# Performance work log

Hardware: AMD Instinct MI355X
Metric: run time of the kernel (lower is better)

The kernel has to match this reference:

```python
import jax, jax.numpy as jnp
import numpy as np

D_MODEL = 768
N_HEADS = 8
HEAD_DIM = D_MODEL // N_HEADS
LN_EPS = 1e-5

def setup_inputs() -> dict:
    key = jax.random.key(0)
    k1, k2, k3 = jax.random.split(key, 3)
    B, L = 8, 4096
    x = jax.random.normal(k1, (B, L, D_MODEL), dtype=jnp.float32)
    gamma = jnp.ones((D_MODEL,), dtype=jnp.float32)
    beta = jnp.zeros((D_MODEL,), dtype=jnp.float32)
    # torch Linear weights transposed so forward is x @ W
    w_qkv = jax.random.normal(k2, (D_MODEL, 3 * D_MODEL), dtype=jnp.float32) * (1.0 / np.sqrt(D_MODEL))
    w_out = jax.random.normal(k3, (D_MODEL, D_MODEL), dtype=jnp.float32) * (1.0 / np.sqrt(D_MODEL))
    return {"x": x, "gamma": gamma, "beta": beta, "w_qkv": w_qkv, "w_out": w_out}

def reference(x, gamma, beta, w_qkv, w_out):
    B, L, D = x.shape
    residual = x
    # LayerNorm
    mu = jnp.mean(x, axis=-1, keepdims=True)
    var = jnp.mean(jnp.square(x - mu), axis=-1, keepdims=True)
    xn = (x - mu) * jax.lax.rsqrt(var + LN_EPS) * gamma + beta
    # qkv projection, split, reshape to [B, H, L, d]
    qkv = xn @ w_qkv  # [B, L, 3D]
    q, k, v = jnp.split(qkv, 3, axis=-1)
    def to_heads(t):
        return t.reshape(B, L, N_HEADS, HEAD_DIM).transpose(0, 2, 1, 3)
    q, k, v = to_heads(q), to_heads(k), to_heads(v)
    # feature maps: elu + 1
    q = jax.nn.elu(q) + 1.0
    k = jax.nn.elu(k) + 1.0
    # linear attention: kv aggregation then query readout
    kv = jnp.einsum('bhld,bhlv->bhdv', k, v)          # [B,H,d,d]
    out = jnp.einsum('bhld,bhdv->bhlv', q, kv)         # [B,H,L,d]
    k_sum = jnp.sum(k, axis=2)                         # [B,H,d]
    normalizer = jnp.einsum('bhld,bhd->bhl', q, k_sum) # [B,H,L]
    normalizer = jnp.maximum(normalizer, 1e-6)
    out = out / normalizer[..., None]
    out = out.transpose(0, 2, 1, 3).reshape(B, L, D)
    out = out @ w_out
    return out + residual
```

## Files before the change

### kernel.cpp

```cpp
#include <hip/hip_runtime.h>
#include <stdint.h>

#define D_MODEL 768
#define N3      2304
#define NHEAD   8
#define DH      96
#define BATCH   8
#define SEQ     4096
#define ROWS    (BATCH*SEQ)
#define LN_EPS  1e-5f

typedef __attribute__((ext_vector_type(8))) __bf16 bf16x8;
typedef __attribute__((ext_vector_type(4))) float f32x4;
typedef __attribute__((ext_vector_type(8))) unsigned short ushort8;
typedef __attribute__((ext_vector_type(4))) unsigned short ushort4v;

__device__ __forceinline__ unsigned short f2bf(float f) {
  union { float f; unsigned int u; } v; v.f = f;
  unsigned int r = v.u + 0x7FFFu + ((v.u >> 16) & 1u);
  return (unsigned short)(r >> 16);
}
__device__ __forceinline__ float bf2f(unsigned short u) {
  union { unsigned int u; float f; } v; v.u = ((unsigned int)u) << 16;
  return v.f;
}

#define GLOBAL_LDS16(src, dst) \
  __builtin_amdgcn_global_load_lds((const __attribute__((address_space(1))) void*)(src), \
                                   (__attribute__((address_space(3))) void*)(dst), 16, 0, 0)

#define GATE(n) do { asm volatile("s_waitcnt vmcnt(" #n ")" ::: "memory"); \
                     __builtin_amdgcn_s_barrier(); asm volatile("" ::: "memory"); } while (0)

__global__ __launch_bounds__(256) void transpose2_kernel(
    const float* __restrict__ wqkv, const float* __restrict__ wout,
    unsigned short* __restrict__ wqkvT, unsigned short* __restrict__ woutT) {
  __shared__ float tile[32][33];
  int bx = blockIdx.x;
  const float* in; unsigned short* out; int C, c0;
  if (bx < 72) { in = wqkv; out = wqkvT; C = N3;      c0 = bx * 32; }
  else         { in = wout; out = woutT; C = D_MODEL; c0 = (bx - 72) * 32; }
  int r0 = blockIdx.y * 32;
  int tx = threadIdx.x & 31, ty = threadIdx.x >> 5;
  #pragma unroll
  for (int i = ty; i < 32; i += 8)
    tile[i][tx] = in[(size_t)(r0 + i) * C + c0 + tx];
  __syncthreads();
  #pragma unroll
  for (int i = ty; i < 32; i += 8)
    out[(size_t)(c0 + i) * D_MODEL + r0 + tx] = f2bf(tile[tx][i]);
}

__global__ __launch_bounds__(256) void ln_kernel(
    const float* __restrict__ x, const float* __restrict__ gamma,
    const float* __restrict__ beta, unsigned short* __restrict__ xn) {
  int wave = threadIdx.x >> 6, lane = threadIdx.x & 63;
  int row = blockIdx.x * 4 + wave;
  const float* xr = x + (size_t)row * D_MODEL;
  f32x4 v[3];
  float s = 0.f, sq = 0.f;
  #pragma unroll
  for (int i = 0; i < 3; ++i) {
    v[i] = *(const f32x4*)(xr + (i * 64 + lane) * 4);
    #pragma unroll
    for (int c = 0; c < 4; ++c) { s += v[i][c]; sq += v[i][c] * v[i][c]; }
  }
  #pragma unroll
  for (int o = 32; o; o >>= 1) {
    s  += __shfl_xor(s, o, 64);
    sq += __shfl_xor(sq, o, 64);
  }
  float mu  = s * (1.f / 768.f);
  float var = sq * (1.f / 768.f) - mu * mu;
  float rs  = rsqrtf(var + LN_EPS);
  #pragma unroll
  for (int i = 0; i < 3; ++i) {
    int col = (i * 64 + lane) * 4;
    ushort4v o;
    #pragma unroll
    for (int c = 0; c < 4; ++c)
      o[c] = f2bf((v[i][c] - mu) * rs * gamma[col + c] + beta[col + c]);
    *(ushort4v*)(xn + (size_t)row * D_MODEL + col) = o;
  }
}

__global__ __launch_bounds__(256, 2) void gemm_qkv_w_kernel(
    const unsigned short* __restrict__ A, const unsigned short* __restrict__ Bt,
    unsigned short* __restrict__ qb, unsigned short* __restrict__ kT,
    unsigned short* __restrict__ vT) {
  __shared__ unsigned short As[3 * 4096];
  __shared__ unsigned short Bs[3 * 8192];
  const int K = D_MODEL, nbn = 9;
  int nwg = gridDim.x, id = blockIdx.x;
  int q8 = nwg >> 3;
  int wg = (id & 7) * q8 + (id >> 3);
  int bm = wg / nbn, bn = wg % nbn;

  const int lane = threadIdx.x & 63, wid = threadIdx.x >> 6;
  const int wn = wid;
  const int l15 = lane & 15, hi = lane >> 4;
  const int colS = (hi ^ ((l15 >> 1) & 3)) << 3;
  const int srow = lane >> 2;
  const int scol = ((lane & 3) ^ ((lane >> 3) & 3)) << 3;

  const unsigned short* a0 = A  + (size_t)(bm * 128 +      wid * 16 + srow) * K + scol;
  const unsigned short* a1 = A  + (size_t)(bm * 128 + 64 + wid * 16 + srow) * K + scol;
  const unsigned short* b0 = Bt + (size_t)(bn * 256 + wid * 64 +      srow) * K + scol;
  const unsigned short* b1 = Bt + (size_t)(bn * 256 + wid * 64 + 16 + srow) * K + scol;
  const unsigned short* b2 = Bt + (size_t)(bn * 256 + wid * 64 + 32 + srow) * K + scol;
  const unsigned short* b3 = Bt + (size_t)(bn * 256 + wid * 64 + 48 + srow) * K + scol;
  auto stage = [&](int buf, int kt) {
    GLOBAL_LDS16(a0 + kt * 32, &As[buf * 4096 +        wid * 512]);
    GLOBAL_LDS16(a1 + kt * 32, &As[buf * 4096 + 2048 + wid * 512]);
    GLOBAL_LDS16(b0 + kt * 32, &Bs[buf * 8192 + wid * 2048]);
    GLOBAL_LDS16(b1 + kt * 32, &Bs[buf * 8192 + wid * 2048 + 512]);
    GLOBAL_LDS16(b2 + kt * 32, &Bs[buf * 8192 + wid * 2048 + 1024]);
    GLOBAL_LDS16(b3 + kt * 32, &Bs[buf * 8192 + wid * 2048 + 1536]);
  };

  f32x4 acc[8][4];
  #pragma unroll
  for (int i = 0; i < 8; ++i)
    #pragma unroll
    for (int j = 0; j < 4; ++j) acc[i][j] = (f32x4){0.f, 0.f, 0.f, 0.f};

#define QTILE(BUF, STG) do { \
    bf16x8 af[8], bv[4]; \
    _Pragma("unroll") for (int mf = 0; mf < 8; ++mf) \
      af[mf] = *(const bf16x8*)&As[(BUF) * 4096 + (mf * 16 + l15) * 32 + colS]; \
    _Pragma("unroll") for (int nf = 0; nf < 4; ++nf) \
      bv[nf] = *(const bf16x8*)&Bs[(BUF) * 8192 + (wn * 64 + nf * 16 + l15) * 32 + colS]; \
    STG; \
    __builtin_amdgcn_s_setprio(1); \
    _Pragma("unroll") for (int mf = 0; mf < 8; ++mf) \
      _Pragma("unroll") for (int nf = 0; nf < 4; ++nf) \
        acc[mf][nf] = __builtin_amdgcn_mfma_f32_16x16x32_bf16( \
            af[mf], bv[nf], acc[mf][nf], 0, 0, 0); \
    __builtin_amdgcn_s_setprio(0); \
  } while (0)

  stage(0, 0); stage(1, 1);
  for (int it = 0; it < 7; ++it) {
    int T = 3 * it;
    GATE(6); QTILE(0, stage(2, T + 2));
    GATE(6); QTILE(1, stage(0, T + 3));
    GATE(6); QTILE(2, stage(1, T + 4));
  }
  GATE(6); QTILE(0, stage(2, 23));
  GATE(6); QTILE(1, {});
  GATE(0); QTILE(2, {});
#undef QTILE

  int r0 = bm * 128, c0 = bn * 256 + wn * 64;
  if (bn < 3) {
    #pragma unroll
    for (int mf = 0; mf < 8; ++mf)
      #pragma unroll
      for (int nf = 0; nf < 4; ++nf) {
        int col = c0 + nf * 16 + l15;
        #pragma unroll
        for (int r = 0; r < 4; ++r) {
          int row = r0 + mf * 16 + hi * 4 + r;
          float v = acc[mf][nf][r];
          v = (v > 0.f) ? v + 1.f : __expf(v);
          qb[(size_t)row * D_MODEL + col] = f2bf(v);
        }
      }
  } else {
    const bool isK = (bn < 6);
    unsigned short* T = isK ? kT : vT;
    int cbase = c0 - (isK ? 768 : 1536);
    #pragma unroll
    for (int mf = 0; mf < 8; ++mf) {
      int ll = mf * 16 + hi * 4;
      #pragma unroll
      for (int nf = 0; nf < 4; ++nf) {
        int cc = cbase + nf * 16 + l15;
        int h = cc / 96, d = cc - h * 96;
        ushort4v pk;
        #pragma unroll
        for (int r = 0; r < 4; ++r) {
          float v = acc[mf][nf][r];
          if (isK) v = (v > 0.f) ? v + 1.f : __expf(v);
          pk[r] = f2bf(v);
        }
        *(ushort4v*)&T[(((size_t)bm * 8 + h) * 96 + d) * 128 + ll] = pk;
      }
    }
  }
}

__global__ __launch_bounds__(256, 3) void gemm_out_kernel(
    const unsigned short* __restrict__ A, const unsigned short* __restrict__ Bt,
    const float* __restrict__ resid, float* __restrict__ Cf) {
  __shared__ unsigned short As[3 * 4096];
  __shared__ unsigned short Bs[3 * 4096];
  const int K = D_MODEL, nbn = 6;
  int nwg = gridDim.x, id = blockIdx.x;
  int q8 = nwg >> 3;
  int wg = (id & 7) * q8 + (id >> 3);
  int bm = wg / nbn, bn = wg % nbn;

  const int lane = threadIdx.x & 63, wid = threadIdx.x >> 6;
  const int wm = wid >> 1, wn = wid & 1;
  const int l15 = lane & 15, hi = lane >> 4;
  const int colS = (hi ^ ((l15 >> 1) & 3)) << 3;
  const int srow = lane >> 2;
  const int scol = ((lane & 3) ^ ((lane >> 3) & 3)) << 3;

  const unsigned short* a0 = A  + (size_t)(bm * 128 +      wid * 16 + srow) * K + scol;
  const unsigned short* a1 = A  + (size_t)(bm * 128 + 64 + wid * 16 + srow) * K + scol;
  const unsigned short* b0 = Bt + (size_t)(bn * 128 +      wid * 16 + srow) * K + scol;
  const unsigned short* b1 = Bt + (size_t)(bn * 128 + 64 + wid * 16 + srow) * K + scol;
  auto stage = [&](int buf, int kt) {
    GLOBAL_LDS16(a0 + kt * 32, &As[buf * 4096 +        wid * 512]);
    GLOBAL_LDS16(a1 + kt * 32, &As[buf * 4096 + 2048 + wid * 512]);
    GLOBAL_LDS16(b0 + kt * 32, &Bs[buf * 4096 +        wid * 512]);
    GLOBAL_LDS16(b1 + kt * 32, &Bs[buf * 4096 + 2048 + wid * 512]);
  };

  f32x4 acc[4][4];
  #pragma unroll
  for (int i = 0; i < 4; ++i)
    #pragma unroll
    for (int j = 0; j < 4; ++j) acc[i][j] = (f32x4){0.f, 0.f, 0.f, 0.f};

#define HTILE(BUF, STG) do { \
    bf16x8 af[4], bv[4]; \
    _Pragma("unroll") for (int mf = 0; mf < 4; ++mf) \
      af[mf] = *(const bf16x8*)&As[(BUF) * 4096 + (wm * 64 + mf * 16 + l15) * 32 + colS]; \
    _Pragma("unroll") for (int nf = 0; nf < 4; ++nf) \
      bv[nf] = *(const bf16x8*)&Bs[(BUF) * 4096 + (wn * 64 + nf * 16 + l15) * 32 + colS]; \
    STG; \
    __builtin_amdgcn_s_setprio(1); \
    _Pragma("unroll") for (int mf = 0; mf < 4; ++mf) \
      _Pragma("unroll") for (int nf = 0; nf < 4; ++nf) \
        acc[mf][nf] = __builtin_amdgcn_mfma_f32_16x16x32_bf16( \
            af[mf], bv[nf], acc[mf][nf], 0, 0, 0); \
    __builtin_amdgcn_s_setprio(0); \
  } while (0)

  stage(0, 0); stage(1, 1);
  for (int it = 0; it < 7; ++it) {
    int T = 3 * it;
    GATE(4); HTILE(0, stage(2, T + 2));
    GATE(4); HTILE(1, stage(0, T + 3));
    GATE(4); HTILE(2, stage(1, T + 4));
  }
  GATE(4); HTILE(0, stage(2, 23));
  GATE(4); HTILE(1, {});
  GATE(0); HTILE(2, {});
#undef HTILE

  int r0 = bm * 128 + wm * 64, c0 = bn * 128 + wn * 64;
  #pragma unroll
  for (int mf = 0; mf < 4; ++mf)
    #pragma unroll
    for (int nf = 0; nf < 4; ++nf) {
      int col = c0 + nf * 16 + l15;
      #pragma unroll
      for (int r = 0; r < 4; ++r) {
        int row = r0 + mf * 16 + hi * 4 + r;
        Cf[(size_t)row * D_MODEL + col] =
            acc[mf][nf][r] + resid[(size_t)row * D_MODEL + col];
      }
    }
}

__global__ __launch_bounds__(256) void kvagg2_kernel(
    const unsigned short* __restrict__ kT, const unsigned short* __restrict__ vT,
    float* __restrict__ kvp) {
  __shared__ unsigned short KTs[3 * 6144];
  __shared__ unsigned short VTs[3 * 8192];
  int bh = blockIdx.x >> 2, chunk = blockIdx.x & 3;
  int tid = threadIdx.x;
  int lane = tid & 63, wid = tid >> 6;
  int l15 = lane & 15, hi = lane >> 4;

  #pragma unroll
  for (int i = 0; i < 3; ++i) {
    int s = i * 256 + tid;
    int buf = s >> 8, r = 96 + ((s >> 3) & 31), sl = s & 7;
    unsigned short val = (r == 96) ? (unsigned short)0x3F80 : (unsigned short)0;
    ushort8 v8 = {val, val, val, val, val, val, val, val};
    *(ushort8*)&VTs[buf * 8192 + r * 64 + sl * 8] = v8;
  }
  __syncthreads();

  const int b = bh >> 3, h = bh & 7;
  auto stage = [&](int buf, int t) {
    #pragma unroll
    for (int i = 0; i < 3; ++i) {
      int sidx = i * 256 + tid;
      int row = sidx >> 3;
      int L = (sidx & 7) ^ (row & 7);
      size_t g = ((((size_t)b * 32 + chunk * 8 + (t >> 1)) * 8 + h) * 96 + row) * 128
               + (t & 1) * 64 + L * 8;
      GLOBAL_LDS16(kT + g, &KTs[buf * 6144 + (i * 256 + wid * 64) * 8]);
      GLOBAL_LDS16(vT + g, &VTs[buf * 8192 + (i * 256 + wid * 64) * 8]);
    }
  };

  f32x4 acc[6][2];
  #pragma unroll
  for (int i = 0; i < 6; ++i)
    #pragma unroll
    for (int j = 0; j < 2; ++j) acc[i][j] = (f32x4){0.f, 0.f, 0.f, 0.f};

#define KVTILE(BUF) do { \
    _Pragma("unroll") for (int kq = 0; kq < 2; ++kq) { \
      bf16x8 af[6], bv[2]; \
      _Pragma("unroll") for (int mf = 0; mf < 6; ++mf) { \
        int row = mf * 16 + l15; \
        af[mf] = *(const bf16x8*)&KTs[(BUF) * 6144 + row * 64 + ((kq * 4 + hi) ^ (row & 7)) * 8]; } \
      _Pragma("unroll") for (int nf = 0; nf < 2; ++nf) { \
        int row = wid * 32 + nf * 16 + l15; \
        bv[nf] = *(const bf16x8*)&VTs[(BUF) * 8192 + row * 64 + ((kq * 4 + hi) ^ (row & 7)) * 8]; } \
      __builtin_amdgcn_s_setprio(1); \
      _Pragma("unroll") for (int mf = 0; mf < 6; ++mf) \
        _Pragma("unroll") for (int nf = 0; nf < 2; ++nf) \
          acc[mf][nf] = __builtin_amdgcn_mfma_f32_16x16x32_bf16( \
              af[mf], bv[nf], acc[mf][nf], 0, 0, 0); \
      __builtin_amdgcn_s_setprio(0); \
    } } while (0)

  stage(0, 0); stage(1, 1);
  for (int t = 0; t < 14; ++t) {
    stage((t + 2) % 3, t + 2);
    GATE(12);
    KVTILE(t % 3);
  }
  GATE(6); KVTILE(2);
  GATE(0); KVTILE(0);
#undef KVTILE

  float* outp = kvp + ((size_t)bh * 4 + chunk) * (96 * 112);
  #pragma unroll
  for (int nf = 0; nf < 2; ++nf) {
    int e = wid * 32 + nf * 16 + l15;
    if (e < 112) {
      #pragma unroll
      for (int mf = 0; mf < 6; ++mf)
        #pragma unroll
        for (int r = 0; r < 4; ++r) {
          int d = mf * 16 + hi * 4 + r;
          outp[d * 112 + e] = acc[mf][nf][r];
        }
    }
  }
}

__global__ __launch_bounds__(256) void kvreduce_kernel(
    const float* __restrict__ kvp, unsigned short* __restrict__ kvTo) {
  int idx = blockIdx.x * 256 + threadIdx.x;
  if (idx >= 64 * 112 * 96) return;
  int d = idx % 96;
  int e = (idx / 96) % 112;
  int bh = idx / (96 * 112);
  float s = 0.f;
  #pragma unroll
  for (int c = 0; c < 4; ++c)
    s += kvp[(((size_t)bh * 4 + c) * 96 + d) * 112 + e];
  kvTo[idx] = f2bf(s);
}

__global__ __launch_bounds__(256) void readout_kernel(
    const unsigned short* __restrict__ qb, const unsigned short* __restrict__ kvT,
    unsigned short* __restrict__ attn) {
  __shared__ unsigned short Qs[128][104];
  __shared__ unsigned short Ks[112][104];
  int bh = blockIdx.x >> 5, lc = blockIdx.x & 31;
  int b = bh >> 3, h = bh & 7;
  int l0 = lc * 128;
  int wave = threadIdx.x >> 6, lane = threadIdx.x & 63;
  #pragma unroll
  for (int i = 0; i < 6; ++i) {
    int idx = i * 256 + threadIdx.x;
    int l = idx / 12, oc = idx % 12;
    size_t g = ((size_t)b * SEQ + l0 + l) * D_MODEL + h * DH + oc * 8;
    *(ushort8*)&Qs[l][oc * 8] = *(const ushort8*)(qb + g);
  }
  const unsigned short* kvbh = kvT + (size_t)bh * 112 * 96;
  #pragma unroll
  for (int i = 0; i < 6; ++i) {
    int idx = i * 256 + threadIdx.x;
    if (idx < 1344) {
      int e = idx / 12, oc = idx % 12;
      *(ushort8*)&Ks[e][oc * 8] = *(const ushort8*)(kvbh + e * 96 + oc * 8);
    }
  }
  __syncthreads();
  f32x4 acc[2][7];
  #pragma unroll
  for (int i = 0; i < 2; ++i)
    #pragma unroll
    for (int j = 0; j < 7; ++j) acc[i][j] = (f32x4){0.f, 0.f, 0.f, 0.f};
  #pragma unroll
  for (int kq = 0; kq < 3; ++kq) {
    int k0 = kq * 32 + (lane >> 4) * 8;
    bf16x8 af[2], bfv[7];
    #pragma unroll
    for (int i = 0; i < 2; ++i) af[i]  = *(const bf16x8*)&Qs[wave * 32 + i * 16 + (lane & 15)][k0];
    #pragma unroll
    for (int j = 0; j < 7; ++j) bfv[j] = *(const bf16x8*)&Ks[j * 16 + (lane & 15)][k0];
    #pragma unroll
    for (int i = 0; i < 2; ++i)
      #pragma unroll
      for (int j = 0; j < 7; ++j)
        acc[i][j] = __builtin_amdgcn_mfma_f32_16x16x32_bf16(af[i], bfv[j], acc[i][j], 0, 0, 0);
  }
  int g4 = lane >> 4;
  #pragma unroll
  for (int i = 0; i < 2; ++i) {
    #pragma unroll
    for (int r = 0; r < 4; ++r) {
      float nv = __shfl(acc[i][6][r], lane & 48, 64);
      float inv = 1.f / fmaxf(nv, 1e-6f);
      size_t orow = (size_t)b * SEQ + l0 + wave * 32 + i * 16 + g4 * 4 + r;
      #pragma unroll
      for (int j = 0; j < 6; ++j) {
        int col = h * DH + j * 16 + (lane & 15);
        attn[orow * D_MODEL + col] = f2bf(acc[i][j][r] * inv);
      }
    }
  }
}

extern "C" void kernel_launch(void* const* d_in, const int* in_sizes, int n_in,
                              void* d_out, int out_size, void* d_ws, size_t ws_size,
                              hipStream_t stream) {
  const float* x     = (const float*)d_in[0];
  const float* gamma = (const float*)d_in[1];
  const float* beta  = (const float*)d_in[2];
  const float* w_qkv = (const float*)d_in[3];
  const float* w_out = (const float*)d_in[4];
  float* out = (float*)d_out;

  char* ws = (char*)d_ws;
  size_t off = 0;
  auto alloc = [&](size_t bytes) -> void* {
    void* p = ws + off; off += (bytes + 255) & ~(size_t)255; return p;
  };
  unsigned short* xn    = (unsigned short*)alloc((size_t)ROWS * D_MODEL * 2);
  unsigned short* qb    = (unsigned short*)alloc((size_t)ROWS * D_MODEL * 2);
  unsigned short* kTb   = (unsigned short*)alloc((size_t)64 * 96 * SEQ * 2);
  unsigned short* vTb   = (unsigned short*)alloc((size_t)64 * 96 * SEQ * 2);
  unsigned short* wqkvT = (unsigned short*)alloc((size_t)N3 * D_MODEL * 2);
  unsigned short* woutT = (unsigned short*)alloc((size_t)D_MODEL * D_MODEL * 2);
  float* kvp            = (float*)alloc((size_t)256 * 96 * 112 * 4);
  unsigned short* kvT   = (unsigned short*)alloc((size_t)64 * 112 * 96 * 2);

  transpose2_kernel<<<dim3(96, 24), 256, 0, stream>>>(w_qkv, w_out, wqkvT, woutT);
  ln_kernel<<<ROWS / 4, 256, 0, stream>>>(x, gamma, beta, xn);
  gemm_qkv_w_kernel<<<(ROWS / 128) * (N3 / 256), 256, 0, stream>>>(xn, wqkvT, qb, kTb, vTb);
  kvagg2_kernel<<<256, 256, 0, stream>>>(kTb, vTb, kvp);
  kvreduce_kernel<<<(64 * 112 * 96 + 255) / 256, 256, 0, stream>>>(kvp, kvT);
  readout_kernel<<<2048, 256, 0, stream>>>(qb, kvT, xn);
  gemm_out_kernel<<<(ROWS / 128) * (D_MODEL / 128), 256, 0, stream>>>(xn, woutT, x, out);
}
```

Before: 326.0 us.

## Fold kv state into output projection per batch, replacing readout GEMM

The per-head kv matrices are premultiplied with the output projection weights, giving a per-batch 768x768 matrix M. Queries are then scaled by their normalizer in a lightweight elementwise kernel, and one GEMM per batch (q_hat @ M + residual) replaces the separate readout GEMM and output GEMM. This removes one full pass over the attention intermediate and the readout MFMA work. In exchange it adds a small premultiply kernel and an extra bf16 rounding of the normalized queries and of M. The final GEMM also moves to a larger 128x256 tile at lower occupancy.

```diff
diff --git a/kernel.cpp b/kernel.cpp
--- a/kernel.cpp
+++ b/kernel.cpp
@@ -188,83 +188,6 @@
       }
     }
   }
-}
-
-__global__ __launch_bounds__(256, 3) void gemm_out_kernel(
-    const unsigned short* __restrict__ A, const unsigned short* __restrict__ Bt,
-    const float* __restrict__ resid, float* __restrict__ Cf) {
-  __shared__ unsigned short As[3 * 4096];
-  __shared__ unsigned short Bs[3 * 4096];
-  const int K = D_MODEL, nbn = 6;
-  int nwg = gridDim.x, id = blockIdx.x;
-  int q8 = nwg >> 3;
-  int wg = (id & 7) * q8 + (id >> 3);
-  int bm = wg / nbn, bn = wg % nbn;
-
-  const int lane = threadIdx.x & 63, wid = threadIdx.x >> 6;
-  const int wm = wid >> 1, wn = wid & 1;
-  const int l15 = lane & 15, hi = lane >> 4;
-  const int colS = (hi ^ ((l15 >> 1) & 3)) << 3;
-  const int srow = lane >> 2;
-  const int scol = ((lane & 3) ^ ((lane >> 3) & 3)) << 3;
-
-  const unsigned short* a0 = A  + (size_t)(bm * 128 +      wid * 16 + srow) * K + scol;
-  const unsigned short* a1 = A  + (size_t)(bm * 128 + 64 + wid * 16 + srow) * K + scol;
-  const unsigned short* b0 = Bt + (size_t)(bn * 128 +      wid * 16 + srow) * K + scol;
-  const unsigned short* b1 = Bt + (size_t)(bn * 128 + 64 + wid * 16 + srow) * K + scol;
-  auto stage = [&](int buf, int kt) {
-    GLOBAL_LDS16(a0 + kt * 32, &As[buf * 4096 +        wid * 512]);
-    GLOBAL_LDS16(a1 + kt * 32, &As[buf * 4096 + 2048 + wid * 512]);
-    GLOBAL_LDS16(b0 + kt * 32, &Bs[buf * 4096 +        wid * 512]);
-    GLOBAL_LDS16(b1 + kt * 32, &Bs[buf * 4096 + 2048 + wid * 512]);
-  };
-
-  f32x4 acc[4][4];
-  #pragma unroll
-  for (int i = 0; i < 4; ++i)
-    #pragma unroll
-    for (int j = 0; j < 4; ++j) acc[i][j] = (f32x4){0.f, 0.f, 0.f, 0.f};
-
-#define HTILE(BUF, STG) do { \
-    bf16x8 af[4], bv[4]; \
-    _Pragma("unroll") for (int mf = 0; mf < 4; ++mf) \
-      af[mf] = *(const bf16x8*)&As[(BUF) * 4096 + (wm * 64 + mf * 16 + l15) * 32 + colS]; \
-    _Pragma("unroll") for (int nf = 0; nf < 4; ++nf) \
-      bv[nf] = *(const bf16x8*)&Bs[(BUF) * 4096 + (wn * 64 + nf * 16 + l15) * 32 + colS]; \
-    STG; \
-    __builtin_amdgcn_s_setprio(1); \
-    _Pragma("unroll") for (int mf = 0; mf < 4; ++mf) \
-      _Pragma("unroll") for (int nf = 0; nf < 4; ++nf) \
-        acc[mf][nf] = __builtin_amdgcn_mfma_f32_16x16x32_bf16( \
-            af[mf], bv[nf], acc[mf][nf], 0, 0, 0); \
-    __builtin_amdgcn_s_setprio(0); \
-  } while (0)
-
-  stage(0, 0); stage(1, 1);
-  for (int it = 0; it < 7; ++it) {
-    int T = 3 * it;
-    GATE(4); HTILE(0, stage(2, T + 2));
-    GATE(4); HTILE(1, stage(0, T + 3));
-    GATE(4); HTILE(2, stage(1, T + 4));
-  }
-  GATE(4); HTILE(0, stage(2, 23));
-  GATE(4); HTILE(1, {});
-  GATE(0); HTILE(2, {});
-#undef HTILE
-
-  int r0 = bm * 128 + wm * 64, c0 = bn * 128 + wn * 64;
-  #pragma unroll
-  for (int mf = 0; mf < 4; ++mf)
-    #pragma unroll
-    for (int nf = 0; nf < 4; ++nf) {
-      int col = c0 + nf * 16 + l15;
-      #pragma unroll
-      for (int r = 0; r < 4; ++r) {
-        int row = r0 + mf * 16 + hi * 4 + r;
-        Cf[(size_t)row * D_MODEL + col] =
-            acc[mf][nf][r] + resid[(size_t)row * D_MODEL + col];
-      }
-    }
 }
 
 __global__ __launch_bounds__(256) void kvagg2_kernel(
@@ -350,80 +273,196 @@
   }
 }
 
-__global__ __launch_bounds__(256) void kvreduce_kernel(
-    const float* __restrict__ kvp, unsigned short* __restrict__ kvTo) {
+__global__ __launch_bounds__(256) void kvreduce2_kernel(
+    const float* __restrict__ kvp, unsigned short* __restrict__ kvN,
+    float* __restrict__ ksumf) {
   int idx = blockIdx.x * 256 + threadIdx.x;
-  if (idx >= 64 * 112 * 96) return;
-  int d = idx % 96;
-  int e = (idx / 96) % 112;
-  int bh = idx / (96 * 112);
+  if (idx >= 64 * 96 * 112) return;
+  int e = idx % 112;
+  int d = (idx / 112) % 96;
+  int bh = idx / (112 * 96);
   float s = 0.f;
   #pragma unroll
   for (int c = 0; c < 4; ++c)
     s += kvp[(((size_t)bh * 4 + c) * 96 + d) * 112 + e];
-  kvTo[idx] = f2bf(s);
-}
-
-__global__ __launch_bounds__(256) void readout_kernel(
-    const unsigned short* __restrict__ qb, const unsigned short* __restrict__ kvT,
-    unsigned short* __restrict__ attn) {
-  __shared__ unsigned short Qs[128][104];
-  __shared__ unsigned short Ks[112][104];
-  int bh = blockIdx.x >> 5, lc = blockIdx.x & 31;
-  int b = bh >> 3, h = bh & 7;
-  int l0 = lc * 128;
-  int wave = threadIdx.x >> 6, lane = threadIdx.x & 63;
-  #pragma unroll
-  for (int i = 0; i < 6; ++i) {
-    int idx = i * 256 + threadIdx.x;
-    int l = idx / 12, oc = idx % 12;
-    size_t g = ((size_t)b * SEQ + l0 + l) * D_MODEL + h * DH + oc * 8;
-    *(ushort8*)&Qs[l][oc * 8] = *(const ushort8*)(qb + g);
-  }
-  const unsigned short* kvbh = kvT + (size_t)bh * 112 * 96;
-  #pragma unroll
-  for (int i = 0; i < 6; ++i) {
-    int idx = i * 256 + threadIdx.x;
-    if (idx < 1344) {
-      int e = idx / 12, oc = idx % 12;
-      *(ushort8*)&Ks[e][oc * 8] = *(const ushort8*)(kvbh + e * 96 + oc * 8);
-    }
+  if (e < 96)       kvN[((size_t)bh * 96 + d) * 96 + e] = f2bf(s);
+  else if (e == 96) ksumf[(size_t)bh * 96 + d] = s;
+}
+
+__global__ __launch_bounds__(256) void mpre_kernel(
+    const unsigned short* __restrict__ kvN, const unsigned short* __restrict__ woutT,
+    unsigned short* __restrict__ Mt) {
+  int bx = blockIdx.x;
+  int cb = bx % 3, h = (bx / 3) % 8, b = bx / 24;
+  int bh = b * 8 + h;
+  const int lane = threadIdx.x & 63, wid = threadIdx.x >> 6;
+  const int l15 = lane & 15, hi = lane >> 4;
+
+  f32x4 acc[6][4];
+  #pragma unroll
+  for (int i = 0; i < 6; ++i)
+    #pragma unroll
+    for (int j = 0; j < 4; ++j) acc[i][j] = (f32x4){0.f, 0.f, 0.f, 0.f};
+
+  #pragma unroll
+  for (int kq = 0; kq < 3; ++kq) {
+    int e = kq * 32 + hi * 8;
+    bf16x8 af[6], bv[4];
+    #pragma unroll
+    for (int rf = 0; rf < 6; ++rf) {
+      int d = rf * 16 + l15;
+      af[rf] = *(const bf16x8*)&kvN[((size_t)bh * 96 + d) * 96 + e];
+    }
+    #pragma unroll
+    for (int cf = 0; cf < 4; ++cf) {
+      int c = cb * 256 + wid * 64 + cf * 16 + l15;
+      bv[cf] = *(const bf16x8*)&woutT[(size_t)c * 768 + h * 96 + e];
+    }
+    #pragma unroll
+    for (int rf = 0; rf < 6; ++rf)
+      #pragma unroll
+      for (int cf = 0; cf < 4; ++cf)
+        acc[rf][cf] = __builtin_amdgcn_mfma_f32_16x16x32_bf16(
+            af[rf], bv[cf], acc[rf][cf], 0, 0, 0);
+  }
+
+  #pragma unroll
+  for (int rf = 0; rf < 6; ++rf) {
+    int hd = h * 96 + rf * 16 + hi * 4;
+    #pragma unroll
+    for (int cf = 0; cf < 4; ++cf) {
+      int c = cb * 256 + wid * 64 + cf * 16 + l15;
+      ushort4v pk;
+      #pragma unroll
+      for (int r = 0; r < 4; ++r) pk[r] = f2bf(acc[rf][cf][r]);
+      *(ushort4v*)&Mt[(size_t)b * 589824 + (size_t)c * 768 + hd] = pk;
+    }
+  }
+}
+
+__global__ __launch_bounds__(256) void scale_kernel(
+    const unsigned short* __restrict__ qb, const float* __restrict__ ksumf,
+    unsigned short* __restrict__ qhat) {
+  __shared__ float ks[8][96];
+  int tid = threadIdx.x;
+  int row0 = blockIdx.x * 64;
+  int b = row0 >> 12;
+  #pragma unroll
+  for (int i = 0; i < 3; ++i) {
+    int idx = i * 256 + tid;
+    if (idx < 768) ks[idx / 96][idx % 96] = ksumf[(size_t)b * 768 + idx];
   }
   __syncthreads();
-  f32x4 acc[2][7];
-  #pragma unroll
-  for (int i = 0; i < 2; ++i)
-    #pragma unroll
-    for (int j = 0; j < 7; ++j) acc[i][j] = (f32x4){0.f, 0.f, 0.f, 0.f};
-  #pragma unroll
-  for (int kq = 0; kq < 3; ++kq) {
-    int k0 = kq * 32 + (lane >> 4) * 8;
-    bf16x8 af[2], bfv[7];
-    #pragma unroll
-    for (int i = 0; i < 2; ++i) af[i]  = *(const bf16x8*)&Qs[wave * 32 + i * 16 + (lane & 15)][k0];
-    #pragma unroll
-    for (int j = 0; j < 7; ++j) bfv[j] = *(const bf16x8*)&Ks[j * 16 + (lane & 15)][k0];
-    #pragma unroll
-    for (int i = 0; i < 2; ++i)
-      #pragma unroll
-      for (int j = 0; j < 7; ++j)
-        acc[i][j] = __builtin_amdgcn_mfma_f32_16x16x32_bf16(af[i], bfv[j], acc[i][j], 0, 0, 0);
-  }
-  int g4 = lane >> 4;
-  #pragma unroll
-  for (int i = 0; i < 2; ++i) {
-    #pragma unroll
-    for (int r = 0; r < 4; ++r) {
-      float nv = __shfl(acc[i][6][r], lane & 48, 64);
-      float inv = 1.f / fmaxf(nv, 1e-6f);
-      size_t orow = (size_t)b * SEQ + l0 + wave * 32 + i * 16 + g4 * 4 + r;
-      #pragma unroll
-      for (int j = 0; j < 6; ++j) {
-        int col = h * DH + j * 16 + (lane & 15);
-        attn[orow * D_MODEL + col] = f2bf(acc[i][j][r] * inv);
+
+  int row = row0 + (tid >> 2), seg = tid & 3;
+  size_t base = (size_t)row * D_MODEL + seg * 192;
+  ushort8 qreg[24];
+  #pragma unroll
+  for (int c = 0; c < 24; ++c)
+    qreg[c] = *(const ushort8*)(qb + base + c * 8);
+
+  float inv[2];
+  #pragma unroll
+  for (int hh = 0; hh < 2; ++hh) {
+    int h = seg * 2 + hh;
+    float n = 0.f;
+    #pragma unroll
+    for (int c = 0; c < 12; ++c)
+      #pragma unroll
+      for (int j = 0; j < 8; ++j)
+        n += bf2f(qreg[hh * 12 + c][j]) * ks[h][c * 8 + j];
+    inv[hh] = 1.f / fmaxf(n, 1e-6f);
+  }
+  #pragma unroll
+  for (int c = 0; c < 24; ++c) {
+    float sc = inv[c / 12];
+    ushort8 o;
+    #pragma unroll
+    for (int j = 0; j < 8; ++j) o[j] = f2bf(bf2f(qreg[c][j]) * sc);
+    *(ushort8*)(qhat + base + c * 8) = o;
+  }
+}
+
+__global__ __launch_bounds__(256, 2) void gemm_fin_kernel(
+    const unsigned short* __restrict__ A, const unsigned short* __restrict__ MtAll,
+    const float* __restrict__ resid, float* __restrict__ Cf) {
+  __shared__ unsigned short As[3 * 4096];
+  __shared__ unsigned short Bs[3 * 8192];
+  const int K = D_MODEL, nbn = 3;
+  int nwg = gridDim.x, id = blockIdx.x;
+  int q8 = nwg >> 3;
+  int wg = (id & 7) * q8 + (id >> 3);
+  int bm = wg / nbn, bn = wg % nbn;
+  const unsigned short* Bt = MtAll + (size_t)(bm >> 5) * 589824;
+
+  const int lane = threadIdx.x & 63, wid = threadIdx.x >> 6;
+  const int wn = wid;
+  const int l15 = lane & 15, hi = lane >> 4;
+  const int colS = (hi ^ ((l15 >> 1) & 3)) << 3;
+  const int srow = lane >> 2;
+  const int scol = ((lane & 3) ^ ((lane >> 3) & 3)) << 3;
+
+  const unsigned short* a0 = A  + (size_t)(bm * 128 +      wid * 16 + srow) * K + scol;
+  const unsigned short* a1 = A  + (size_t)(bm * 128 + 64 + wid * 16 + srow) * K + scol;
+  const unsigned short* b0 = Bt + (size_t)(bn * 256 + wid * 64 +      srow) * K + scol;
+  const unsigned short* b1 = Bt + (size_t)(bn * 256 + wid * 64 + 16 + srow) * K + scol;
+  const unsigned short* b2 = Bt + (size_t)(bn * 256 + wid * 64 + 32 + srow) * K + scol;
+  const unsigned short* b3 = Bt + (size_t)(bn * 256 + wid * 64 + 48 + srow) * K + scol;
+  auto stage = [&](int buf, int kt) {
+    GLOBAL_LDS16(a0 + kt * 32, &As[buf * 4096 +        wid * 512]);
+    GLOBAL_LDS16(a1 + kt * 32, &As[buf * 4096 + 2048 + wid * 512]);
+    GLOBAL_LDS16(b0 + kt * 32, &Bs[buf * 8192 + wid * 2048]);
+    GLOBAL_LDS16(b1 + kt * 32, &Bs[buf * 8192 + wid * 2048 + 512]);
+    GLOBAL_LDS16(b2 + kt * 32, &Bs[buf * 8192 + wid * 2048 + 1024]);
+    GLOBAL_LDS16(b3 + kt * 32, &Bs[buf * 8192 + wid * 2048 + 1536]);
+  };
+
+  f32x4 acc[8][4];
+  #pragma unroll
+  for (int i = 0; i < 8; ++i)
+    #pragma unroll
+    for (int j = 0; j < 4; ++j) acc[i][j] = (f32x4){0.f, 0.f, 0.f, 0.f};
+
+#define FTILE(BUF, STG) do { \
+    bf16x8 af[8], bv[4]; \
+    _Pragma("unroll") for (int mf = 0; mf < 8; ++mf) \
+      af[mf] = *(const bf16x8*)&As[(BUF) * 4096 + (mf * 16 + l15) * 32 + colS]; \
+    _Pragma("unroll") for (int nf = 0; nf < 4; ++nf) \
+      bv[nf] = *(const bf16x8*)&Bs[(BUF) * 8192 + (wn * 64 + nf * 16 + l15) * 32 + colS]; \
+    STG; \
+    __builtin_amdgcn_s_setprio(1); \
+    _Pragma("unroll") for (int mf = 0; mf < 8; ++mf) \
+      _Pragma("unroll") for (int nf = 0; nf < 4; ++nf) \
+        acc[mf][nf] = __builtin_amdgcn_mfma_f32_16x16x32_bf16( \
+            af[mf], bv[nf], acc[mf][nf], 0, 0, 0); \
+    __builtin_amdgcn_s_setprio(0); \
+  } while (0)
+
+  stage(0, 0); stage(1, 1);
+  for (int it = 0; it < 7; ++it) {
+    int T = 3 * it;
+    GATE(6); FTILE(0, stage(2, T + 2));
+    GATE(6); FTILE(1, stage(0, T + 3));
+    GATE(6); FTILE(2, stage(1, T + 4));
+  }
+  GATE(6); FTILE(0, stage(2, 23));
+  GATE(6); FTILE(1, {});
+  GATE(0); FTILE(2, {});
+#undef FTILE
+
+  int r0 = bm * 128, c0 = bn * 256 + wn * 64;
+  #pragma unroll
+  for (int mf = 0; mf < 8; ++mf)
+    #pragma unroll
+    for (int nf = 0; nf < 4; ++nf) {
+      int col = c0 + nf * 16 + l15;
+      #pragma unroll
+      for (int r = 0; r < 4; ++r) {
+        int row = r0 + mf * 16 + hi * 4 + r;
+        Cf[(size_t)row * D_MODEL + col] =
+            acc[mf][nf][r] + resid[(size_t)row * D_MODEL + col];
       }
     }
-  }
 }
 
 extern "C" void kernel_launch(void* const* d_in, const int* in_sizes, int n_in,
@@ -448,13 +487,16 @@
   unsigned short* wqkvT = (unsigned short*)alloc((size_t)N3 * D_MODEL * 2);
   unsigned short* woutT = (unsigned short*)alloc((size_t)D_MODEL * D_MODEL * 2);
   float* kvp            = (float*)alloc((size_t)256 * 96 * 112 * 4);
-  unsigned short* kvT   = (unsigned short*)alloc((size_t)64 * 112 * 96 * 2);
+  unsigned short* kvN   = (unsigned short*)alloc((size_t)64 * 96 * 96 * 2);
+  float* ksumf          = (float*)alloc((size_t)64 * 96 * 4);
+  unsigned short* Mt    = (unsigned short*)alloc((size_t)BATCH * 768 * 768 * 2);
 
   transpose2_kernel<<<dim3(96, 24), 256, 0, stream>>>(w_qkv, w_out, wqkvT, woutT);
   ln_kernel<<<ROWS / 4, 256, 0, stream>>>(x, gamma, beta, xn);
   gemm_qkv_w_kernel<<<(ROWS / 128) * (N3 / 256), 256, 0, stream>>>(xn, wqkvT, qb, kTb, vTb);
   kvagg2_kernel<<<256, 256, 0, stream>>>(kTb, vTb, kvp);
-  kvreduce_kernel<<<(64 * 112 * 96 + 255) / 256, 256, 0, stream>>>(kvp, kvT);
-  readout_kernel<<<2048, 256, 0, stream>>>(qb, kvT, xn);
-  gemm_out_kernel<<<(ROWS / 128) * (D_MODEL / 128), 256, 0, stream>>>(xn, woutT, x, out);
-}
+  kvreduce2_kernel<<<(64 * 96 * 112 + 255) / 256, 256, 0, stream>>>(kvp, kvN, ksumf);
+  mpre_kernel<<<192, 256, 0, stream>>>(kvN, woutT, Mt);
+  scale_kernel<<<ROWS / 64, 256, 0, stream>>>(qb, ksumf, xn);
+  gemm_fin_kernel<<<(ROWS / 128) * 3, 256, 0, stream>>>(xn, Mt, x, out);
+}
```

Measured after the change: 328.2 us. No clear change (+0.7%).
